# Kernel optimization log

Hardware: AMD Instinct MI355X
Metric: run time of the kernel (lower is better)

The kernel has to match this reference:

```python
import jax, jax.numpy as jnp
import numpy as np

R = 16            # search_range
D = 2 * R + 1     # 33 offsets per axis -> 1089 cost channels
B, C, H, W = 64, 256, 16, 16
OUT = 512         # conv channels for search_range=16
FULLY = 1024
EPS_BN = 1e-5
EPS_NORM = 1e-12
LRELU_SLOPE = 0.01


def l2_normalize(x):
    # torch F.normalize(x, dim=1, p=2): x / clamp_min(||x||_2, 1e-12)
    n = jnp.sqrt(jnp.sum(x * x, axis=1, keepdims=True))
    return x / jnp.maximum(n, EPS_NORM)


def cost_volume(c1, warp, r):
    # Fused equivalent of the original (2r+1)^2 Python-loop of slice/mul/mean:
    # one dense correlation GEMM over the padded map, then a gather of the
    # diagonal-band entries. cost[b,dy,dx,i,j] = mean_c c1[b,c,i,j]*pad[b,c,i+dy,j+dx]
    b, c, h, w = c1.shape
    d = 2 * r + 1
    padded = jnp.pad(warp, ((0, 0), (0, 0), (r, r), (r, r)))          # (B,C,h+2r,w+2r)
    full = jnp.einsum('bcij,bcuv->bijuv', c1, padded) / c             # (B,h,w,h+2r,w+2r)
    dy = jnp.arange(d)
    ii = jnp.arange(h)
    jj = jnp.arange(w)
    I = ii[None, None, :, None]                 # (1,1,h,1)
    J = jj[None, None, None, :]                 # (1,1,1,w)
    U = dy[:, None, None, None] + I             # (d,1,h,1)
    V = dy[None, :, None, None] + J             # (1,d,1,w)
    cost = full[:, I, J, U, V]                  # (B,d,d,h,w)
    cost = cost.reshape(b, d * d, h, w)
    return jnp.where(cost > 0, cost, LRELU_SLOPE * cost)  # LeakyReLU(0.01)


def conv_bn_relu(x, Wc, bc, g, be, stride):
    y = jax.lax.conv_general_dilated(
        x, Wc, window_strides=(stride, stride), padding=((1, 1), (1, 1)),
        dimension_numbers=('NCHW', 'OIHW', 'NCHW'))
    y = y + bc[None, :, None, None]
    # training-mode BatchNorm: biased batch stats over (B,H,W)
    mu = jnp.mean(y, axis=(0, 2, 3), keepdims=True)
    var = jnp.var(y, axis=(0, 2, 3), keepdims=True)
    y = (y - mu) * jax.lax.rsqrt(var + EPS_BN)
    y = y * g[None, :, None, None] + be[None, :, None, None]
    return jnp.maximum(y, 0.0)


def setup_inputs() -> dict:
    key = jax.random.key(0)
    ks = jax.random.split(key, 10)
    s = 0.02
    inp = {
        'feature1': jax.random.normal(ks[0], (B, C, H, W), jnp.float32),
        'feature2': jax.random.normal(ks[1], (B, C, H, W), jnp.float32),
        'W1': jax.random.normal(ks[2], (OUT, D * D, 3, 3), jnp.float32) * s,
        'b1': jnp.zeros((OUT,), jnp.float32),
        'g1': jnp.ones((OUT,), jnp.float32),
        'be1': jnp.zeros((OUT,), jnp.float32),
        'W2': jax.random.normal(ks[3], (OUT, OUT, 3, 3), jnp.float32) * s,
        'b2': jnp.zeros((OUT,), jnp.float32),
        'g2': jnp.ones((OUT,), jnp.float32),
        'be2': jnp.zeros((OUT,), jnp.float32),
        'W3': jax.random.normal(ks[4], (OUT, OUT, 3, 3), jnp.float32) * s,
        'b3': jnp.zeros((OUT,), jnp.float32),
        'g3': jnp.ones((OUT,), jnp.float32),
        'be3': jnp.zeros((OUT,), jnp.float32),
        'Wf1': jax.random.normal(ks[5], (FULLY, 256 * OUT), jnp.float32) * s,
        'bf1': jnp.zeros((FULLY,), jnp.float32),
        'Wf2': jax.random.normal(ks[6], (8, FULLY), jnp.float32) * s,
        'bf2': jnp.zeros((8,), jnp.float32),
    }
    return inp


def reference(feature1, feature2, W1, b1, g1, be1, W2, b2, g2, be2,
              W3, b3, g3, be3, Wf1, bf1, Wf2, bf2):
    # warped=False: normalize both feature maps
    gc = cost_volume(l2_normalize(feature1), l2_normalize(feature2), R)
    x = conv_bn_relu(gc, W1, b1, g1, be1, 1)
    x = conv_bn_relu(x, W2, b2, g2, be2, 1)
    x = conv_bn_relu(x, W3, b3, g3, be3, 1)
    x = x.reshape(x.shape[0], -1)               # (B, 512*16*16)
    x = jnp.maximum(x @ Wf1.T + bf1, 0.0)       # Linear + ReLU
    # Dropout treated as identity (deterministic reference)
    offset = x @ Wf2.T + bf2                    # (B, 8)
    return offset
```

## Files before the change

### kernel.cpp

```cpp
#include <hip/hip_runtime.h>
#include <hip/hip_bf16.h>
#include <stdint.h>


typedef unsigned short ushort_t;
typedef __attribute__((ext_vector_type(8))) short     bf16x8;
typedef __attribute__((ext_vector_type(8))) unsigned short u16x8;
typedef __attribute__((ext_vector_type(4))) unsigned short u16x4;
typedef __attribute__((ext_vector_type(4))) float     f32x4;

#define NB   64
#define NC   256
#define NP   256
#define KCV  256
#define KP1  1152
#define NOUT 512
#define NROWS 16384
#define KFC  131072
#define NF   1024
#define KSPL 32

__device__ __forceinline__ unsigned short f2bf(float x) {
  union { float f; unsigned u; } c; c.f = x;
  unsigned r = c.u + 0x7FFFu + ((c.u >> 16) & 1u);
  return (unsigned short)(r >> 16);
}
__device__ __forceinline__ float b2f(unsigned short u) {
  union { unsigned u; float f; } c; c.u = ((unsigned)u) << 16; return c.f;
}

__device__ __forceinline__ void gl_lds16(const void* g, void* l) {
  __builtin_amdgcn_global_load_lds(
      (const __attribute__((address_space(1))) unsigned int*)g,
      (__attribute__((address_space(3))) unsigned int*)l, 16, 0, 0);
}

__device__ __forceinline__ f32x4 mfma16(bf16x8 a, bf16x8 b, f32x4 c) {
  return __builtin_amdgcn_mfma_f32_16x16x32_bf16(a, b, c, 0, 0, 0);
}

__global__ __launch_bounds__(256) void l2norm_t(
    const float* __restrict__ f1, const float* __restrict__ f2,
    ushort_t* __restrict__ AT, ushort_t* __restrict__ N2T)
{
  const float* src = blockIdx.y ? f2 : f1;
  ushort_t*    dst = blockIdx.y ? N2T : AT;
  const int b = blockIdx.x, t = threadIdx.x;
  const float* sb = src + (size_t)b * NC * NP;
  float sq = 0.f;
  for (int c = 0; c < NC; ++c) { float v = sb[c * NP + t]; sq += v * v; }
  float sc = 1.f / fmaxf(sqrtf(sq), 1e-12f);
  ushort_t* db = dst + ((size_t)b * NP + t) * NC;
  for (int c0 = 0; c0 < NC; c0 += 8) {
    u16x8 pk;
#pragma unroll
    for (int q = 0; q < 8; ++q) pk[q] = f2bf(sb[(c0 + q) * NP + t] * sc);
    *(u16x8*)(db + c0) = pk;
  }
}

__global__ __launch_bounds__(256) void pack_w(
    const float* __restrict__ W, ushort_t* __restrict__ Wp,
    int Cin, int Kp, int total)
{
  int p = blockIdx.x * 256 + threadIdx.x;
  if (p >= total) return;
  int tap = p / (NOUT * Kp);
  int rem = p - tap * (NOUT * Kp);
  int o   = rem / Kp;
  int cin = rem - o * Kp;
  float v = (cin < Cin) ? W[((size_t)o * Cin + cin) * 9 + tap] : 0.f;
  Wp[p] = f2bf(v);
}

__global__ __launch_bounds__(256) void cv_gemm(
    const ushort_t* __restrict__ AT,
    const ushort_t* __restrict__ N2T,
    ushort_t* __restrict__ costT,
    const ushort_t* __restrict__ zerot)
{
  __shared__ ushort_t As[128 * 64];
  __shared__ ushort_t Bs[128 * 64];
  const int tid = threadIdx.x, lane = tid & 63, wave = tid >> 6;
  const int wr = wave >> 1, wc = wave & 1;
  const int la = lane & 15, lb = lane >> 4;
  const int b  = blockIdx.z;
  const int m0 = blockIdx.y * 128;
  const int n0 = blockIdx.x * 128;

  {
    const int iMin = blockIdx.y * 8, iMax = iMin + 7;
    const int uMin = n0 / 48, uMax = (n0 + 127) / 48;
    if (uMax < iMin || uMin > iMax + 32) return;
  }

  f32x4 acc[4][4];
#pragma unroll
  for (int i = 0; i < 4; ++i)
#pragma unroll
    for (int j = 0; j < 4; ++j) acc[i][j] = (f32x4){0.f, 0.f, 0.f, 0.f};

  const ushort_t* srcA[4];
  const ushort_t* srcB[4];
#pragma unroll
  for (int s = 0; s < 4; ++s) {
    int idx = tid + (s << 8);
    int row = idx >> 3, c16 = idx & 7;
    srcA[s] = AT + ((size_t)b * NP + m0 + row) * NC + c16 * 8;
    int uv = n0 + row;
    int u = uv / 48, v = uv - u * 48;
    int oi = u - 16, oj = v - 16;
    bool val = ((unsigned)oi < 16u) & ((unsigned)oj < 16u);
    srcB[s] = val ? (N2T + ((size_t)b * NP + oi * 16 + oj) * NC + c16 * 8)
                  : (const ushort_t*)0;
  }

  for (int kc = 0; kc < KCV; kc += 64) {
#pragma unroll
    for (int s = 0; s < 4; ++s) {
      int idx = tid + (s << 8);
      gl_lds16(srcA[s] + kc, &As[idx * 8]);
      const ushort_t* g = srcB[s] ? srcB[s] + kc : zerot;
      gl_lds16(g, &Bs[idx * 8]);
    }
    __syncthreads();
#pragma unroll
    for (int kk = 0; kk < 2; ++kk) {
      bf16x8 af[4], bfv[4];
#pragma unroll
      for (int mi = 0; mi < 4; ++mi)
        af[mi] = *(const bf16x8*)&As[(wr * 64 + mi * 16 + la) * 64 + kk * 32 + lb * 8];
#pragma unroll
      for (int ni = 0; ni < 4; ++ni)
        bfv[ni] = *(const bf16x8*)&Bs[(wc * 64 + ni * 16 + la) * 64 + kk * 32 + lb * 8];
#pragma unroll
      for (int mi = 0; mi < 4; ++mi)
#pragma unroll
        for (int ni = 0; ni < 4; ++ni)
          acc[mi][ni] = mfma16(af[mi], bfv[ni], acc[mi][ni]);
    }
    __syncthreads();
  }

  const float sc = 1.f / 256.f;
#pragma unroll
  for (int ni = 0; ni < 4; ++ni) {
    int uv = n0 + wc * 64 + ni * 16 + la;
    int u = uv / 48, v = uv - u * 48;
#pragma unroll
    for (int mi = 0; mi < 4; ++mi) {
      int ij = m0 + wr * 64 + mi * 16 + lb * 4;
#pragma unroll
      for (int r = 0; r < 4; ++r) {
        int ijr = ij + r;
        int i = ijr >> 4, j = ijr & 15;
        int dy = u - i, dx = v - j;
        if ((unsigned)dy < 33u && (unsigned)dx < 33u) {
          float vv = acc[mi][ni][r] * sc;
          vv = vv > 0.f ? vv : 0.01f * vv;
          costT[((size_t)b * NP + ijr) * KP1 + dy * 33 + dx] = f2bf(vv);
        }
      }
    }
  }
}

__global__ __launch_bounds__(512, 1) void conv_gemm256(
    const ushort_t* __restrict__ X, const ushort_t* __restrict__ Wp,
    const float* __restrict__ bias, ushort_t* __restrict__ Y0,
    ushort_t* __restrict__ Y1, const int K, const int TPT, const int NT2,
    const ushort_t* __restrict__ zerot)
{
  __shared__ ushort_t lds[65536];
  const int tid = threadIdx.x;
  const int lane = tid & 63, wave = tid >> 6;
  const int wr = wave >> 2, wc = wave & 3;
  const int la = lane & 15, lb = lane >> 4;

  const int bid = blockIdx.x;
  const int L = ((bid & 7) << 5) + (bid >> 3);
  const int g = L >> 7;
  const int rem = L & 127;
  const int b = rem >> 1;
  const int n0 = (rem & 1) << 8;
  const int t0 = g * NT2;

  int amask[4];
  const ushort_t* abase[4];
  const ushort_t* bbase[4];
#pragma unroll
  for (int s = 0; s < 4; ++s) {
    int idx = tid + (s << 9);
    int ks = idx & 7, loc = (idx >> 3) & 63;
    int rA = ((s & 1) << 7) + ((s >> 1) << 6) + loc;
    int i = rA >> 4, j = rA & 15;
    int m = 0;
#pragma unroll
    for (int tap = 0; tap < 9; ++tap) {
      int i2 = i + tap / 3 - 1, j2 = j + tap % 3 - 1;
      if (((unsigned)i2 < 16u) & ((unsigned)j2 < 16u)) m |= 1 << tap;
    }
    amask[s] = m;
    abase[s] = X + (size_t)(b * NP + rA) * K + ((ks ^ (rA & 7)) << 3);
    int rB = ((s & 1) << 7) + ((loc >> 5) << 6) + ((s >> 1) << 5) + (loc & 31);
    bbase[s] = Wp + (size_t)(n0 + rB) * K + ((ks ^ (rB & 7)) << 3);
  }

  const int ck0 = ((0 + lb) ^ (la & 7)) << 3;
  const int ck1 = ((4 + lb) ^ (la & 7)) << 3;
  const int a_base = wr * 4096 + la * 64;
  const int b_base = 16384 + (wc >> 1) * 4096 + (wc & 1) * 2048 + la * 64;

  f32x4 acc[8][4];
#pragma unroll
  for (int i = 0; i < 8; ++i)
#pragma unroll
    for (int j = 0; j < 4; ++j) acc[i][j] = (f32x4){0.f, 0.f, 0.f, 0.f};

  auto tile_par = [&](int tg, int& toffA, size_t& wtap, int& tap) {
    tap = tg / TPT;
    int kc = (tg - tap * TPT) << 6;
    int ty = tap / 3;
    toffA = (ty * 16 + (tap - 3 * ty) - 17) * K + kc;
    wtap  = (size_t)tap * NOUT * K + kc;
  };

#define STAGE_A(S) { const ushort_t* gp = ((amask[S] >> tapN) & 1) ? abase[S] + toffN : zerot; \
                     gl_lds16(gp, &bufn[(tid + ((S) << 9)) * 8]); }
#define STAGE_B(S) gl_lds16(bbase[S] + wtapN, &bufn[16384 + (tid + ((S) << 9)) * 8]);

#define READ_A03() \
  Af[0][0] = *(const bf16x8*)&buf[a_base + 0    + ck0]; Af[0][1] = *(const bf16x8*)&buf[a_base + 0    + ck1]; \
  Af[1][0] = *(const bf16x8*)&buf[a_base + 1024 + ck0]; Af[1][1] = *(const bf16x8*)&buf[a_base + 1024 + ck1]; \
  Af[2][0] = *(const bf16x8*)&buf[a_base + 2048 + ck0]; Af[2][1] = *(const bf16x8*)&buf[a_base + 2048 + ck1]; \
  Af[3][0] = *(const bf16x8*)&buf[a_base + 3072 + ck0]; Af[3][1] = *(const bf16x8*)&buf[a_base + 3072 + ck1];
#define READ_A47() \
  Af[4][0] = *(const bf16x8*)&buf[a_base + 8192 + 0    + ck0]; Af[4][1] = *(const bf16x8*)&buf[a_base + 8192 + 0    + ck1]; \
  Af[5][0] = *(const bf16x8*)&buf[a_base + 8192 + 1024 + ck0]; Af[5][1] = *(const bf16x8*)&buf[a_base + 8192 + 1024 + ck1]; \
  Af[6][0] = *(const bf16x8*)&buf[a_base + 8192 + 2048 + ck0]; Af[6][1] = *(const bf16x8*)&buf[a_base + 8192 + 2048 + ck1]; \
  Af[7][0] = *(const bf16x8*)&buf[a_base + 8192 + 3072 + ck0]; Af[7][1] = *(const bf16x8*)&buf[a_base + 8192 + 3072 + ck1];
#define READ_B(NOFF) \
  bf00 = *(const bf16x8*)&buf[b_base + (NOFF) + 0    + ck0]; bf01 = *(const bf16x8*)&buf[b_base + (NOFF) + 0    + ck1]; \
  bf10 = *(const bf16x8*)&buf[b_base + (NOFF) + 1024 + ck0]; bf11 = *(const bf16x8*)&buf[b_base + (NOFF) + 1024 + ck1];
#define MFMA_QUAD(MB, N0, N1) \
  acc[MB+0][N0] = mfma16(Af[MB+0][0], bf00, acc[MB+0][N0]); \
  acc[MB+0][N1] = mfma16(Af[MB+0][0], bf10, acc[MB+0][N1]); \
  acc[MB+1][N0] = mfma16(Af[MB+1][0], bf00, acc[MB+1][N0]); \
  acc[MB+1][N1] = mfma16(Af[MB+1][0], bf10, acc[MB+1][N1]); \
  acc[MB+2][N0] = mfma16(Af[MB+2][0], bf00, acc[MB+2][N0]); \
  acc[MB+2][N1] = mfma16(Af[MB+2][0], bf10, acc[MB+2][N1]); \
  acc[MB+3][N0] = mfma16(Af[MB+3][0], bf00, acc[MB+3][N0]); \
  acc[MB+3][N1] = mfma16(Af[MB+3][0], bf10, acc[MB+3][N1]); \
  acc[MB+0][N0] = mfma16(Af[MB+0][1], bf01, acc[MB+0][N0]); \
  acc[MB+0][N1] = mfma16(Af[MB+0][1], bf11, acc[MB+0][N1]); \
  acc[MB+1][N0] = mfma16(Af[MB+1][1], bf01, acc[MB+1][N0]); \
  acc[MB+1][N1] = mfma16(Af[MB+1][1], bf11, acc[MB+1][N1]); \
  acc[MB+2][N0] = mfma16(Af[MB+2][1], bf01, acc[MB+2][N0]); \
  acc[MB+2][N1] = mfma16(Af[MB+2][1], bf11, acc[MB+2][N1]); \
  acc[MB+3][N0] = mfma16(Af[MB+3][1], bf01, acc[MB+3][N0]); \
  acc[MB+3][N1] = mfma16(Af[MB+3][1], bf11, acc[MB+3][N1]);

  {
    ushort_t* bufn = &lds[0];
    int tapN, toffN; size_t wtapN;
    tile_par(t0, toffN, wtapN, tapN);
    STAGE_A(0) STAGE_A(1) STAGE_A(2) STAGE_A(3)
    STAGE_B(0) STAGE_B(1) STAGE_B(2) STAGE_B(3)
  }
  asm volatile("s_waitcnt vmcnt(2)" ::: "memory");
  __builtin_amdgcn_s_barrier();

  bf16x8 Af[8][2];

  for (int t = 0; t < NT2 - 1; ++t) {
    const ushort_t* buf = &lds[(t & 1) << 15];
    ushort_t* bufn = &lds[((t + 1) & 1) << 15];
    int tapN, toffN; size_t wtapN;
    tile_par(t0 + t + 1, toffN, wtapN, tapN);
    bf16x8 bf00, bf01, bf10, bf11;

    READ_A03()
    READ_B(0)
    STAGE_A(0) STAGE_A(1)
    asm volatile("s_waitcnt vmcnt(6)" ::: "memory");
    __builtin_amdgcn_s_barrier();
    asm volatile("s_waitcnt lgkmcnt(0)" ::: "memory");
    __builtin_amdgcn_sched_barrier(0);
    __builtin_amdgcn_s_setprio(1);
    MFMA_QUAD(0, 0, 1)
    __builtin_amdgcn_s_setprio(0);

    READ_A47()
    READ_B(0)
    STAGE_A(2) STAGE_A(3)
    asm volatile("s_waitcnt vmcnt(4)" ::: "memory");
    __builtin_amdgcn_s_barrier();
    asm volatile("s_waitcnt lgkmcnt(0)" ::: "memory");
    __builtin_amdgcn_sched_barrier(0);
    __builtin_amdgcn_s_setprio(1);
    MFMA_QUAD(4, 0, 1)
    __builtin_amdgcn_s_setprio(0);

    READ_B(8192)
    STAGE_B(0) STAGE_B(1)
    __builtin_amdgcn_s_barrier();
    asm volatile("s_waitcnt lgkmcnt(0)" ::: "memory");
    __builtin_amdgcn_sched_barrier(0);
    __builtin_amdgcn_s_setprio(1);
    MFMA_QUAD(0, 2, 3)
    __builtin_amdgcn_s_setprio(0);

    READ_B(8192)
    STAGE_B(2) STAGE_B(3)
    asm volatile("s_waitcnt vmcnt(2)" ::: "memory");
    __builtin_amdgcn_s_barrier();
    asm volatile("s_waitcnt lgkmcnt(0)" ::: "memory");
    __builtin_amdgcn_sched_barrier(0);
    __builtin_amdgcn_s_setprio(1);
    MFMA_QUAD(4, 2, 3)
    __builtin_amdgcn_s_setprio(0);
  }

  {
    const ushort_t* buf = &lds[((NT2 - 1) & 1) << 15];
    bf16x8 bf00, bf01, bf10, bf11;
    asm volatile("s_waitcnt vmcnt(0)" ::: "memory");
    __builtin_amdgcn_s_barrier();
    READ_A03()
    READ_B(0)
    asm volatile("s_waitcnt lgkmcnt(0)" ::: "memory");
    __builtin_amdgcn_sched_barrier(0);
    MFMA_QUAD(0, 0, 1)
    READ_A47()
    asm volatile("s_waitcnt lgkmcnt(0)" ::: "memory");
    __builtin_amdgcn_sched_barrier(0);
    MFMA_QUAD(4, 0, 1)
    READ_B(8192)
    asm volatile("s_waitcnt lgkmcnt(0)" ::: "memory");
    __builtin_amdgcn_sched_barrier(0);
    MFMA_QUAD(0, 2, 3)
    MFMA_QUAD(4, 2, 3)
  }

  ushort_t* Yh = g ? Y1 : Y0;
#pragma unroll
  for (int ni = 0; ni < 4; ++ni) {
    int col = n0 + wc * 64 + ni * 16 + la;
    float bv = 0.5f * bias[col];
#pragma unroll
    for (int mi = 0; mi < 8; ++mi) {
      int row = b * NP + wr * 128 + mi * 16 + lb * 4;
#pragma unroll
      for (int r = 0; r < 4; ++r)
        Yh[(size_t)(row + r) * NOUT + col] = f2bf(acc[mi][ni][r] + bv);
    }
  }
#undef STAGE_A
#undef STAGE_B
#undef READ_A03
#undef READ_A47
#undef READ_B
#undef MFMA_QUAD
}

__global__ __launch_bounds__(512) void bn_stat2(
    const ushort_t* __restrict__ Y0, const ushort_t* __restrict__ Y1,
    float* __restrict__ st)
{
  const int col = threadIdx.x;
  const size_t base = (size_t)blockIdx.x * 32 * NOUT;
  float s = 0.f, q = 0.f;
  for (int r = 0; r < 32; ++r) {
    float y = b2f(Y0[base + r * NOUT + col]) + b2f(Y1[base + r * NOUT + col]);
    s += y; q += y * y;
  }
  atomicAdd(&st[col], s);
  atomicAdd(&st[512 + col], q);
}

__global__ __launch_bounds__(256) void bn_apply2(
    const ushort_t* __restrict__ Y0, const ushort_t* __restrict__ Y1,
    const float* __restrict__ st, const float* __restrict__ g,
    const float* __restrict__ be, ushort_t* __restrict__ Xo)
{
  const size_t idx = (size_t)blockIdx.x * 256 + threadIdx.x;
  u16x8 a = *(const u16x8*)(Y0 + idx * 8);
  u16x8 c = *(const u16x8*)(Y1 + idx * 8);
  const int c0 = (int)((idx * 8) & 511);
  u16x8 pk;
#pragma unroll
  for (int q = 0; q < 8; ++q) {
    int cc = c0 + q;
    float y = b2f(a[q]) + b2f(c[q]);
    float mu  = st[cc] * (1.f / 16384.f);
    float var = st[512 + cc] * (1.f / 16384.f) - mu * mu;
    float s = rsqrtf(var + 1e-5f) * g[cc];
    pk[q] = f2bf(fmaxf((y - mu) * s + be[cc], 0.f));
  }
  *(u16x8*)(Xo + idx * 8) = pk;
}

__global__ __launch_bounds__(256) void bn_apply2_t(
    const ushort_t* __restrict__ Y0, const ushort_t* __restrict__ Y1,
    const float* __restrict__ st, const float* __restrict__ g,
    const float* __restrict__ be, ushort_t* __restrict__ Xf)
{
  __shared__ ushort_t T[64][65];
  const int c0  = blockIdx.x * 64;
  const int ij0 = blockIdx.y * 64;
  const int b   = blockIdx.z;
  const int tid = threadIdx.x;

#pragma unroll
  for (int it = 0; it < 16; ++it) {
    int e = it * 256 + tid;
    int ij = e >> 6, c = e & 63;
    int cg = c0 + c;
    size_t off = ((size_t)(b * NP + ij0 + ij)) * NOUT + cg;
    float y = b2f(Y0[off]) + b2f(Y1[off]);
    float mu  = st[cg] * (1.f / 16384.f);
    float var = st[512 + cg] * (1.f / 16384.f) - mu * mu;
    float s = rsqrtf(var + 1e-5f) * g[cg];
    T[ij][c] = f2bf(fmaxf((y - mu) * s + be[cg], 0.f));
  }
  __syncthreads();
#pragma unroll
  for (int it = 0; it < 16; ++it) {
    int e = it * 256 + tid;
    int cr = e >> 6, ijc = e & 63;
    Xf[(size_t)b * KFC + (size_t)(c0 + cr) * NP + ij0 + ijc] = T[ijc][cr];
  }
}

__device__ __forceinline__ u16x8 pack8(float4 a, float4 b) {
  u16x8 r;
  r[0] = f2bf(a.x); r[1] = f2bf(a.y); r[2] = f2bf(a.z); r[3] = f2bf(a.w);
  r[4] = f2bf(b.x); r[5] = f2bf(b.y); r[6] = f2bf(b.z); r[7] = f2bf(b.w);
  return r;
}

__global__ __launch_bounds__(256) void fc1_gemm(
    const ushort_t* __restrict__ Xf, const float* __restrict__ Wf1,
    float* __restrict__ hacc)
{
  __shared__ ushort_t As[64 * 64];
  __shared__ ushort_t Bs[64 * 64];
  const int tid = threadIdx.x, lane = tid & 63, wave = tid >> 6;
  const int la = lane & 15, lb = lane >> 4;
  const int f0 = blockIdx.x * 64;
  const int k0 = blockIdx.y * 4096;

  f32x4 acc[4];
#pragma unroll
  for (int i = 0; i < 4; ++i) acc[i] = (f32x4){0.f, 0.f, 0.f, 0.f};

  const ushort_t* xrow[2];
#pragma unroll
  for (int s = 0; s < 2; ++s) {
    int idx = tid + (s << 8);
    xrow[s] = Xf + (size_t)(idx >> 3) * KFC + k0 + (idx & 7) * 8;
  }
  const int brow = tid >> 2, kseg = (tid & 3) * 16;
  const float* wrow = Wf1 + (size_t)(f0 + brow) * KFC + k0 + kseg;

  for (int kc = 0; kc < 4096; kc += 64) {
#pragma unroll
    for (int s = 0; s < 2; ++s) {
      int idx = tid + (s << 8);
      gl_lds16(xrow[s] + kc, &As[idx * 8]);
    }
    float4 w0 = *(const float4*)(wrow + kc);
    float4 w1 = *(const float4*)(wrow + kc + 4);
    float4 w2 = *(const float4*)(wrow + kc + 8);
    float4 w3 = *(const float4*)(wrow + kc + 12);
    *(u16x8*)&Bs[brow * 64 + kseg]     = pack8(w0, w1);
    *(u16x8*)&Bs[brow * 64 + kseg + 8] = pack8(w2, w3);
    __syncthreads();
#pragma unroll
    for (int kk = 0; kk < 2; ++kk) {
      bf16x8 bfv = *(const bf16x8*)&Bs[(wave * 16 + la) * 64 + kk * 32 + lb * 8];
#pragma unroll
      for (int mi = 0; mi < 4; ++mi) {
        bf16x8 av = *(const bf16x8*)&As[(mi * 16 + la) * 64 + kk * 32 + lb * 8];
        acc[mi] = mfma16(av, bfv, acc[mi]);
      }
    }
    __syncthreads();
  }

  float* slice = hacc + (size_t)blockIdx.y * NB * NF;
#pragma unroll
  for (int mi = 0; mi < 4; ++mi) {
    int row = mi * 16 + lb * 4;
#pragma unroll
    for (int r = 0; r < 4; ++r)
      slice[(size_t)(row + r) * NF + f0 + wave * 16 + la] = acc[mi][r];
  }
}

__global__ __launch_bounds__(256) void fc2_out(
    const float* __restrict__ hacc, const float* __restrict__ bf1,
    const float* __restrict__ Wf2, const float* __restrict__ bf2,
    float* __restrict__ out)
{
  const int b = blockIdx.x, tid = threadIdx.x;
  float a[8];
#pragma unroll
  for (int o = 0; o < 8; ++o) a[o] = 0.f;
  for (int f = tid; f < NF; f += 256) {
    float hv = bf1[f];
#pragma unroll 4
    for (int s = 0; s < KSPL; ++s)
      hv += hacc[((size_t)s * NB + b) * NF + f];
    hv = fmaxf(hv, 0.f);
#pragma unroll
    for (int o = 0; o < 8; ++o) a[o] += hv * Wf2[o * NF + f];
  }
  __shared__ float red[8][256];
#pragma unroll
  for (int o = 0; o < 8; ++o) red[o][tid] = a[o];
  __syncthreads();
  for (int s = 128; s > 0; s >>= 1) {
    if (tid < s) {
#pragma unroll
      for (int o = 0; o < 8; ++o) red[o][tid] += red[o][tid + s];
    }
    __syncthreads();
  }
  if (tid < 8) out[b * 8 + tid] = red[tid][0] + bf2[tid];
}

extern "C" void kernel_launch(void* const* d_in, const int* in_sizes, int n_in,
                              void* d_out, int out_size, void* d_ws, size_t ws_size,
                              hipStream_t stream) {
  const float* f1  = (const float*)d_in[0];
  const float* f2  = (const float*)d_in[1];
  const float* W1  = (const float*)d_in[2];
  const float* b1  = (const float*)d_in[3];
  const float* g1  = (const float*)d_in[4];
  const float* be1 = (const float*)d_in[5];
  const float* W2  = (const float*)d_in[6];
  const float* b2  = (const float*)d_in[7];
  const float* g2  = (const float*)d_in[8];
  const float* be2 = (const float*)d_in[9];
  const float* W3  = (const float*)d_in[10];
  const float* b3  = (const float*)d_in[11];
  const float* g3  = (const float*)d_in[12];
  const float* be3 = (const float*)d_in[13];
  const float* Wf1 = (const float*)d_in[14];
  const float* bf1 = (const float*)d_in[15];
  const float* Wf2 = (const float*)d_in[16];
  const float* bf2 = (const float*)d_in[17];
  float* out = (float*)d_out;

  char* ws = (char*)d_ws;
  size_t off = 0;
  auto alloc = [&](size_t bytes) -> void* {
    void* p = ws + off;
    off += (bytes + 255) & ~(size_t)255;
    return p;
  };

  ushort_t* zerot = (ushort_t*)alloc(256);
  float* st1  = (float*)alloc(1024 * 4);
  float* st2  = (float*)alloc(1024 * 4);
  float* st3  = (float*)alloc(1024 * 4);
  const size_t zero_bytes = off;

  float* hacc = (float*)alloc((size_t)KSPL * NB * NF * 4);
  const size_t SZ_AT   = (size_t)NB * NP * NC * 2;
  const size_t SZ_COST = (size_t)NB * NP * KP1 * 2;
  const size_t SZ_WP1  = (size_t)9 * NOUT * KP1 * 2;
  const size_t SZ_WP23 = (size_t)9 * NOUT * 512 * 2;
  ushort_t* AT    = (ushort_t*)alloc(SZ_AT);
  ushort_t* N2T   = (ushort_t*)alloc(SZ_AT);
  ushort_t* costT = (ushort_t*)alloc(SZ_COST);
  ushort_t* Wp1   = (ushort_t*)alloc(SZ_WP1);
  ushort_t* Wp2   = (ushort_t*)alloc(SZ_WP23);
  ushort_t* Wp3   = (ushort_t*)alloc(SZ_WP23);
  ushort_t* Yh0   = (ushort_t*)alloc((size_t)NROWS * NOUT * 2);
  ushort_t* Yh1   = (ushort_t*)alloc((size_t)NROWS * NOUT * 2);
  ushort_t* Xbuf  = (ushort_t*)alloc((size_t)NROWS * NOUT * 2);
  ushort_t* Xf    = (ushort_t*)alloc((size_t)NB * KFC * 2);

  hipMemsetAsync(ws, 0, zero_bytes, stream);
  hipMemsetAsync(costT, 0, SZ_COST, stream);

  l2norm_t<<<dim3(64, 2), 256, 0, stream>>>(f1, f2, AT, N2T);

  pack_w<<<(9 * NOUT * KP1 + 255) / 256, 256, 0, stream>>>(W1, Wp1, 1089, KP1, 9 * NOUT * KP1);
  pack_w<<<(9 * NOUT * 512 + 255) / 256, 256, 0, stream>>>(W2, Wp2, 512, 512, 9 * NOUT * 512);
  pack_w<<<(9 * NOUT * 512 + 255) / 256, 256, 0, stream>>>(W3, Wp3, 512, 512, 9 * NOUT * 512);

  cv_gemm<<<dim3(18, 2, 64), 256, 0, stream>>>(AT, N2T, costT, zerot);

  conv_gemm256<<<256, 512, 0, stream>>>(costT, Wp1, b1, Yh0, Yh1, KP1, 18, 81, zerot);
  bn_stat2<<<512, 512, 0, stream>>>(Yh0, Yh1, st1);
  bn_apply2<<<4096, 256, 0, stream>>>(Yh0, Yh1, st1, g1, be1, Xbuf);

  conv_gemm256<<<256, 512, 0, stream>>>(Xbuf, Wp2, b2, Yh0, Yh1, 512, 8, 36, zerot);
  bn_stat2<<<512, 512, 0, stream>>>(Yh0, Yh1, st2);
  bn_apply2<<<4096, 256, 0, stream>>>(Yh0, Yh1, st2, g2, be2, Xbuf);

  conv_gemm256<<<256, 512, 0, stream>>>(Xbuf, Wp3, b3, Yh0, Yh1, 512, 8, 36, zerot);
  bn_stat2<<<512, 512, 0, stream>>>(Yh0, Yh1, st3);
  bn_apply2_t<<<dim3(8, 4, 64), 256, 0, stream>>>(Yh0, Yh1, st3, g3, be3, Xf);

  fc1_gemm<<<dim3(16, KSPL), 256, 0, stream>>>(Xf, Wf1, hacc);
  fc2_out<<<64, 256, 0, stream>>>(hacc, bf1, Wf2, bf2, out);

  (void)in_sizes; (void)n_in; (void)out_size; (void)ws_size;
}
```

Measured before the change: 621.2 us.

## Compute compact 256x256 correlation then scatter cost volume in separate pass

Replaces the padded-map correlation GEMM (which ran over a 48x48 padded grid with zero tiles and a band-filter epilogue) with a dense 256x256 per-batch correlation written to an fp32 buffer. A new kernel then gathers each pixel's 1089 offsets from that buffer, applies scale and LeakyReLU, and writes every entry of the cost row, padding included. This removes the memset of the cost buffer and the wasted MFMA work on padding. The three weight-pack launches are merged into one. It adds a 16 MB fp32 intermediate round trip and one extra launch.

```diff
diff --git a/kernel.cpp b/kernel.cpp
--- a/kernel.cpp
+++ b/kernel.cpp
@@ -7,12 +7,12 @@
 typedef __attribute__((ext_vector_type(8))) short     bf16x8;
 typedef __attribute__((ext_vector_type(8))) unsigned short u16x8;
 typedef __attribute__((ext_vector_type(4))) unsigned short u16x4;
+typedef __attribute__((ext_vector_type(2))) unsigned short u16x2;
 typedef __attribute__((ext_vector_type(4))) float     f32x4;
 
 #define NB   64
 #define NC   256
 #define NP   256
-#define KCV  256
 #define KP1  1152
 #define NOUT 512
 #define NROWS 16384
@@ -59,25 +59,31 @@
   }
 }
 
-__global__ __launch_bounds__(256) void pack_w(
-    const float* __restrict__ W, ushort_t* __restrict__ Wp,
-    int Cin, int Kp, int total)
+#define T1P (9 * NOUT * KP1)
+#define T23 (9 * NOUT * 512)
+__global__ __launch_bounds__(256) void pack_all(
+    const float* __restrict__ W1, const float* __restrict__ W2,
+    const float* __restrict__ W3, ushort_t* __restrict__ Wp1,
+    ushort_t* __restrict__ Wp2, ushort_t* __restrict__ Wp3)
 {
   int p = blockIdx.x * 256 + threadIdx.x;
-  if (p >= total) return;
-  int tap = p / (NOUT * Kp);
-  int rem = p - tap * (NOUT * Kp);
+  const float* W; ushort_t* Wp; int Cin, Kp, q;
+  if (p < T1P)            { W = W1; Wp = Wp1; Cin = 1089; Kp = KP1; q = p; }
+  else if (p < T1P + T23) { W = W2; Wp = Wp2; Cin = 512;  Kp = 512; q = p - T1P; }
+  else if (p < T1P + 2 * T23) { W = W3; Wp = Wp3; Cin = 512; Kp = 512; q = p - T1P - T23; }
+  else return;
+  int tap = q / (NOUT * Kp);
+  int rem = q - tap * (NOUT * Kp);
   int o   = rem / Kp;
   int cin = rem - o * Kp;
   float v = (cin < Cin) ? W[((size_t)o * Cin + cin) * 9 + tap] : 0.f;
-  Wp[p] = f2bf(v);
-}
-
-__global__ __launch_bounds__(256) void cv_gemm(
+  Wp[q] = f2bf(v);
+}
+
+__global__ __launch_bounds__(256) void corr_gemm(
     const ushort_t* __restrict__ AT,
     const ushort_t* __restrict__ N2T,
-    ushort_t* __restrict__ costT,
-    const ushort_t* __restrict__ zerot)
+    float* __restrict__ C)
 {
   __shared__ ushort_t As[128 * 64];
   __shared__ ushort_t Bs[128 * 64];
@@ -88,12 +94,6 @@
   const int m0 = blockIdx.y * 128;
   const int n0 = blockIdx.x * 128;
 
-  {
-    const int iMin = blockIdx.y * 8, iMax = iMin + 7;
-    const int uMin = n0 / 48, uMax = (n0 + 127) / 48;
-    if (uMax < iMin || uMin > iMax + 32) return;
-  }
-
   f32x4 acc[4][4];
 #pragma unroll
   for (int i = 0; i < 4; ++i)
@@ -106,22 +106,16 @@
   for (int s = 0; s < 4; ++s) {
     int idx = tid + (s << 8);
     int row = idx >> 3, c16 = idx & 7;
-    srcA[s] = AT + ((size_t)b * NP + m0 + row) * NC + c16 * 8;
-    int uv = n0 + row;
-    int u = uv / 48, v = uv - u * 48;
-    int oi = u - 16, oj = v - 16;
-    bool val = ((unsigned)oi < 16u) & ((unsigned)oj < 16u);
-    srcB[s] = val ? (N2T + ((size_t)b * NP + oi * 16 + oj) * NC + c16 * 8)
-                  : (const ushort_t*)0;
-  }
-
-  for (int kc = 0; kc < KCV; kc += 64) {
+    srcA[s] = AT  + ((size_t)b * NP + m0 + row) * NC + c16 * 8;
+    srcB[s] = N2T + ((size_t)b * NP + n0 + row) * NC + c16 * 8;
+  }
+
+  for (int kc = 0; kc < NC; kc += 64) {
 #pragma unroll
     for (int s = 0; s < 4; ++s) {
       int idx = tid + (s << 8);
       gl_lds16(srcA[s] + kc, &As[idx * 8]);
-      const ushort_t* g = srcB[s] ? srcB[s] + kc : zerot;
-      gl_lds16(g, &Bs[idx * 8]);
+      gl_lds16(srcB[s] + kc, &Bs[idx * 8]);
     }
     __syncthreads();
 #pragma unroll
@@ -142,27 +136,43 @@
     __syncthreads();
   }
 
-  const float sc = 1.f / 256.f;
 #pragma unroll
   for (int ni = 0; ni < 4; ++ni) {
-    int uv = n0 + wc * 64 + ni * 16 + la;
-    int u = uv / 48, v = uv - u * 48;
+    int col = n0 + wc * 64 + ni * 16 + la;
 #pragma unroll
     for (int mi = 0; mi < 4; ++mi) {
-      int ij = m0 + wr * 64 + mi * 16 + lb * 4;
-#pragma unroll
-      for (int r = 0; r < 4; ++r) {
-        int ijr = ij + r;
-        int i = ijr >> 4, j = ijr & 15;
-        int dy = u - i, dx = v - j;
-        if ((unsigned)dy < 33u && (unsigned)dx < 33u) {
-          float vv = acc[mi][ni][r] * sc;
-          vv = vv > 0.f ? vv : 0.01f * vv;
-          costT[((size_t)b * NP + ijr) * KP1 + dy * 33 + dx] = f2bf(vv);
-        }
-      }
-    }
-  }
+      int p = m0 + wr * 64 + mi * 16 + lb * 4;
+#pragma unroll
+      for (int r = 0; r < 4; ++r)
+        C[((size_t)b * NP + p + r) * NP + col] = acc[mi][ni][r];
+    }
+  }
+}
+
+__global__ __launch_bounds__(576) void cost_write(
+    const float* __restrict__ C, ushort_t* __restrict__ costT)
+{
+  __shared__ float row[256];
+  const int ij = blockIdx.x, b = blockIdx.y, tid = threadIdx.x;
+  const float* cr = C + ((size_t)b * NP + ij) * NP;
+  if (tid < 256) row[tid] = cr[tid];
+  __syncthreads();
+  const int i = ij >> 4, j = ij & 15;
+  const int d0 = tid * 2;
+  u16x2 pk;
+#pragma unroll
+  for (int q = 0; q < 2; ++q) {
+    int dd = d0 + q;
+    int dy = dd / 33;
+    int dx = dd - dy * 33;
+    int oi = dy + i - 16, oj = dx + j - 16;
+    float v = 0.f;
+    if (((unsigned)oi < 16u) & ((unsigned)oj < 16u))
+      v = row[oi * 16 + oj] * (1.f / 256.f);
+    v = v > 0.f ? v : 0.01f * v;
+    pk[q] = f2bf(v);
+  }
+  *(u16x2*)(costT + ((size_t)b * NP + ij) * KP1 + d0) = pk;
 }
 
 __global__ __launch_bounds__(512, 1) void conv_gemm256(
@@ -574,6 +584,7 @@
   const size_t SZ_WP23 = (size_t)9 * NOUT * 512 * 2;
   ushort_t* AT    = (ushort_t*)alloc(SZ_AT);
   ushort_t* N2T   = (ushort_t*)alloc(SZ_AT);
+  float*    Cbuf  = (float*)alloc((size_t)NB * NP * NP * 4);
   ushort_t* costT = (ushort_t*)alloc(SZ_COST);
   ushort_t* Wp1   = (ushort_t*)alloc(SZ_WP1);
   ushort_t* Wp2   = (ushort_t*)alloc(SZ_WP23);
@@ -584,15 +595,13 @@
   ushort_t* Xf    = (ushort_t*)alloc((size_t)NB * KFC * 2);
 
   hipMemsetAsync(ws, 0, zero_bytes, stream);
-  hipMemsetAsync(costT, 0, SZ_COST, stream);
 
   l2norm_t<<<dim3(64, 2), 256, 0, stream>>>(f1, f2, AT, N2T);
 
-  pack_w<<<(9 * NOUT * KP1 + 255) / 256, 256, 0, stream>>>(W1, Wp1, 1089, KP1, 9 * NOUT * KP1);
-  pack_w<<<(9 * NOUT * 512 + 255) / 256, 256, 0, stream>>>(W2, Wp2, 512, 512, 9 * NOUT * 512);
-  pack_w<<<(9 * NOUT * 512 + 255) / 256, 256, 0, stream>>>(W3, Wp3, 512, 512, 9 * NOUT * 512);
-
-  cv_gemm<<<dim3(18, 2, 64), 256, 0, stream>>>(AT, N2T, costT, zerot);
+  pack_all<<<(T1P + 2 * T23 + 255) / 256, 256, 0, stream>>>(W1, W2, W3, Wp1, Wp2, Wp3);
+
+  corr_gemm<<<dim3(2, 2, 64), 256, 0, stream>>>(AT, N2T, Cbuf);
+  cost_write<<<dim3(256, 64), 576, 0, stream>>>(Cbuf, costT);
 
   conv_gemm256<<<256, 512, 0, stream>>>(costT, Wp1, b1, Yh0, Yh1, KP1, 18, 81, zerot);
   bn_stat2<<<512, 512, 0, stream>>>(Yh0, Yh1, st1);
```

Result: faster. 607.3 us (-2.2%).
